# Performance work log

Hardware: AMD Instinct MI355X
Metric: run time of the kernel (lower is better)

## Reference

```python
import jax, jax.numpy as jnp
import numpy as np

N, F, P, NT = 4096, 256, 5, 5  # agents, feat dim, n_persona, n_time_steps
EPS = 1e-8


def setup_inputs() -> dict:
    key = jax.random.key(0)
    ks = jax.random.split(key, 7)
    attributes = jax.random.normal(ks[0], (N, F), dtype=jnp.float32)
    edges = (jax.random.uniform(ks[1], (N, N)) < 0.01).astype(jnp.float32)
    persona = jax.random.uniform(ks[2], (NT, N, P), dtype=jnp.float32)
    T = jax.random.uniform(ks[3], (P,), dtype=jnp.float32) * 0.5 + 0.5  # keep temperature away from 0
    e = jax.random.uniform(ks[4], (P,), dtype=jnp.float32) + 0.5
    r = jax.random.uniform(ks[5], (P,), dtype=jnp.float32)
    W = jax.random.uniform(ks[6], (P,), dtype=jnp.float32) + 0.5
    return {"attributes": attributes, "edges": edges, "persona": persona,
            "T": T, "e": e, "r": r, "W": W, "times": 2}


def reference(attributes, edges, persona, T, e, r, W, times):
    p = persona[times]                      # [N, P] persona weights at this time step
    msg = edges @ attributes                # [N, F] message passing, shared across personas

    def body(acc, xs):
        idx, Ti, ei, ri, Wi, pi = xs        # pi: [N]
        feat = ri * attributes + (msg * Wi) * (1.0 - ri)          # [N, F]
        nf = feat / jnp.sqrt(jnp.sum(feat * feat, axis=1, keepdims=True))  # row L2 norm
        x = jnp.exp((nf @ nf.T) / (Ti + EPS)) * ei                 # [N, N]
        x = x / (jnp.max(x) + EPS)                                 # min-max scale (min=0)
        # (1 - exp(-2v)) / (1 + exp(-2v)) == tanh(v)
        tc = jnp.tanh(x) * pi[None, :]                              # column persona gating
        # i == 0 initializes edges_prob with tc, every i adds row-gated tc
        acc = acc + tc * pi[:, None] + jnp.where(idx == 0, 1.0, 0.0) * tc
        return acc, None

    acc0 = jnp.zeros((N, N), dtype=jnp.float32)
    out, _ = jax.lax.scan(body, acc0, (jnp.arange(P), T, e, r, W, p.T))
    return out
```

## Files before the change

### kernel.cpp

```cpp
#include <hip/hip_runtime.h>
#include <hip/hip_bf16.h>

#define N 4096
#define F 256
#define P 5
#define EPSV 1e-8f
#define BK 32
#define NSTEP (F / BK)
#define NTRI 2080
#define GRIDSZ 512
#define DDEG 12
#define NC (DDEG + 1)

typedef __attribute__((ext_vector_type(8))) short bf16x8;
typedef __attribute__((ext_vector_type(4))) float f32x4;
typedef __attribute__((ext_vector_type(2))) float f32x2;

__device__ __forceinline__ f32x4 mfma16(bf16x8 a, bf16x8 b, f32x4 c) {
    return __builtin_amdgcn_mfma_f32_16x16x32_bf16(a, b, c, 0, 0, 0);
}

__device__ __forceinline__ void gload16(const void* src, const char* ldsdst) {
    __builtin_amdgcn_global_load_lds(
        (const __attribute__((address_space(1))) void*)src,
        (__attribute__((address_space(3))) void*)ldsdst, 16, 0, 0);
}

__device__ __forceinline__ f32x2 sp(float x) { return (f32x2){x, x}; }

__global__ __launch_bounds__(256, 8) void prep_kernel(
    const float* __restrict__ E, const float* __restrict__ A,
    const float* __restrict__ persona,
    const float* __restrict__ Tt, const float* __restrict__ ee,
    const float* __restrict__ rr, const float* __restrict__ Ww,
    const int* __restrict__ times,
    __hip_bfloat16* __restrict__ Abf, __hip_bfloat16* __restrict__ Mbf,
    float* __restrict__ qsoa, float* __restrict__ cstg, int* __restrict__ ctr) {
    __shared__ int cnt;
    __shared__ int list[1024];
    const int a = blockIdx.x;
    const int t = threadIdx.x;
    if (t == 0) cnt = 0;
    __syncthreads();
    const float4* erow = (const float4*)(E + (size_t)a * N);
    for (int b = t; b < N / 4; b += 256) {
        const float4 v = erow[b];
        if (v.x != 0.f) list[atomicAdd(&cnt, 1)] = 4 * b;
        if (v.y != 0.f) list[atomicAdd(&cnt, 1)] = 4 * b + 1;
        if (v.z != 0.f) list[atomicAdd(&cnt, 1)] = 4 * b + 2;
        if (v.w != 0.f) list[atomicAdd(&cnt, 1)] = 4 * b + 3;
    }
    __syncthreads();
    const int c = cnt;
    float s0 = 0.f, s1 = 0.f, s2 = 0.f, s3 = 0.f;
    float s4 = 0.f, s5 = 0.f, s6 = 0.f, s7 = 0.f;
    int j = 0;
    for (; j + 8 <= c; j += 8) {
        s0 += A[(size_t)list[j] * F + t];
        s1 += A[(size_t)list[j + 1] * F + t];
        s2 += A[(size_t)list[j + 2] * F + t];
        s3 += A[(size_t)list[j + 3] * F + t];
        s4 += A[(size_t)list[j + 4] * F + t];
        s5 += A[(size_t)list[j + 5] * F + t];
        s6 += A[(size_t)list[j + 6] * F + t];
        s7 += A[(size_t)list[j + 7] * F + t];
    }
    for (; j < c; ++j) s0 += A[(size_t)list[j] * F + t];
    const float mv = ((s0 + s1) + (s2 + s3)) + ((s4 + s5) + (s6 + s7));
    const float av = A[(size_t)a * F + t];
    Abf[(size_t)a * F + t] = __float2bfloat16(av);
    Mbf[(size_t)a * F + t] = __float2bfloat16(mv);

    float paa = av * av, pam = av * mv, pmm = mv * mv;
    #pragma unroll
    for (int o = 32; o > 0; o >>= 1) {
        paa += __shfl_down(paa, o);
        pam += __shfl_down(pam, o);
        pmm += __shfl_down(pmm, o);
    }
    __shared__ float s[3][4];
    const int wid = t >> 6;
    if ((t & 63) == 0) { s[0][wid] = paa; s[1][wid] = pam; s[2][wid] = pmm; }
    __syncthreads();
    if (t < P) {
        const float naa = s[0][0] + s[0][1] + s[0][2] + s[0][3];
        const float nam = s[1][0] + s[1][1] + s[1][2] + s[1][3];
        const float nmm = s[2][0] + s[2][1] + s[2][2] + s[2][3];
        const float Ti = Tt[t], ei = ee[t], ri = rr[t], Wi = Ww[t];
        const float wb = (1.f - ri) * Wi;
        const float n2 = ri * ri * naa + 2.f * ri * wb * nam + wb * wb * nmm;
        const float rn = rsqrtf(n2);
        const float p = persona[(size_t)(*times) * (size_t)N * P + (size_t)a * P + t];
        qsoa[(t * 4 + 0) * N + a] = ri * rn;
        qsoa[(t * 4 + 1) * N + a] = wb * rn;
        qsoa[(t * 4 + 2) * N + a] = p;
        qsoa[(t * 4 + 3) * N + a] = p + (t == 0 ? 1.f : 0.f);
        if (a == 0) {
            const float kk = 1.f / (Ti + EPSV);
            const float scf = ei / (ei * __expf(kk) + EPSV);
            float ch[NC];
            #pragma unroll
            for (int j2 = 0; j2 < NC; ++j2) ch[j2] = 0.f;
            for (int m = 0; m < 32; ++m) {
                const float th = 3.14159265358979323846f * (m + 0.5f) / 32.f;
                const float c1 = __cosf(th);
                const float x = scf * __expf(kk * 1.05f * c1);
                const float e2 = __expf(2.f * x);
                const float fm = 1.f - 2.f / (e2 + 1.f);
                float cjm1 = 1.f, cj = c1;
                ch[0] += fm;
                ch[1] += fm * c1;
                #pragma unroll
                for (int j2 = 2; j2 < NC; ++j2) {
                    const float cn = 2.f * c1 * cj - cjm1;
                    ch[j2] += fm * cn;
                    cjm1 = cj;
                    cj = cn;
                }
            }
            #pragma unroll
            for (int j2 = 0; j2 < NC; ++j2) ch[j2] *= (j2 == 0 ? 1.f : 2.f) / 32.f;
            float mono[NC], Tp[NC], Tc[NC], Tn[NC];
            const float is = 1.f / 1.05f;
            #pragma unroll
            for (int k2 = 0; k2 < NC; ++k2) {
                mono[k2] = 0.f; Tp[k2] = 0.f; Tc[k2] = 0.f; Tn[k2] = 0.f;
            }
            Tp[0] = 1.f;
            Tc[1] = is;
            #pragma unroll
            for (int k2 = 0; k2 < NC; ++k2) mono[k2] += ch[0] * Tp[k2] + ch[1] * Tc[k2];
            for (int j2 = 2; j2 < NC; ++j2) {
                #pragma unroll
                for (int k2 = 0; k2 < NC; ++k2)
                    Tn[k2] = 2.f * is * (k2 ? Tc[k2 - 1] : 0.f) - Tp[k2];
                #pragma unroll
                for (int k2 = 0; k2 < NC; ++k2) mono[k2] += ch[j2] * Tn[k2];
                #pragma unroll
                for (int k2 = 0; k2 < NC; ++k2) { Tp[k2] = Tc[k2]; Tc[k2] = Tn[k2]; }
            }
            #pragma unroll
            for (int k2 = 0; k2 < NC; ++k2) cstg[t * NC + k2] = mono[k2];
        }
    }
    if (a == 0 && t == 0) *ctr = GRIDSZ;
}

__global__ __launch_bounds__(512) void gram_kernel(
    const __hip_bfloat16* __restrict__ Abf, const __hip_bfloat16* __restrict__ Mbf,
    const float* __restrict__ qsoa, const float* __restrict__ cstg,
    int* __restrict__ ctr, float* __restrict__ out) {
    __shared__ __align__(16) char smem[43280];
    __shared__ int snext;

    const int t = threadIdx.x;
    const int lane = t & 63;
    const int w = t >> 6;
    const int wr = w >> 1;
    const int wc = w & 1;

    const int sslot = (lane & 3) ^ ((lane >> 3) & 3);
    const int srowoff = (w & 1) * 32 + (lane >> 2);
    const int ldsp = (w >> 1) * 4096 + (w & 1) * 2048;
    const __hip_bfloat16* smat = ((w >> 1) & 1) ? Mbf : Abf;

    const int frow = lane & 15;
    const int fg = lane >> 4;
    const int jr = fg << 2;
    const int rdslot = (fg ^ ((frow >> 1) & 3)) << 4;
    const int aoff = (wr * 16 + frow) * 64 + rdslot;
    const int coff0 = (wc * 32 + frow) * 64 + rdslot;
    const int coff1 = (wc * 32 + 16 + frow) * 64 + rdslot;

    const float* qlr = (const float*)(smem + 32768);
    const float* qlc = (const float*)(smem + 37888);
    const float* cfs = (const float*)(smem + 43008);

    int raw = blockIdx.x;
    while (raw < NTRI) {
        const int bid = (raw & 7) * 260 + (raw >> 3);
        int bx = (int)((sqrtf(8.f * (float)bid + 1.f) - 1.f) * 0.5f);
        while ((bx + 1) * (bx + 2) / 2 <= bid) ++bx;
        while (bx * (bx + 1) / 2 > bid) --bx;
        const int by = bid - bx * (bx + 1) / 2;
        const int row0 = by << 6, col0 = bx << 6;

        const int sbase = (w < 4) ? row0 : col0;
        const __hip_bfloat16* psrc =
            smat + (size_t)(sbase + srowoff) * F + sslot * 8;

        #define STAGE(b, ks)  do {                                        \
            const char* lb_ = smem + (b) * 16384 + ldsp;                  \
            gload16(psrc + (ks), lb_);                                    \
            gload16(psrc + (ks) + 16 * F, lb_ + 1024);                    \
        } while (0)

        __syncthreads();
        STAGE(0, 0);
        if (w == 0) {
            #pragma unroll
            for (int it = 0; it < 5; ++it)
                gload16(qsoa + (it * 4 + (lane >> 4)) * N + row0 + (lane & 15) * 4,
                        smem + 32768 + it * 1024);
        } else if (w == 1) {
            #pragma unroll
            for (int it = 0; it < 5; ++it)
                gload16(qsoa + (it * 4 + (lane >> 4)) * N + col0 + (lane & 15) * 4,
                        smem + 37888 + it * 1024);
        } else if (w == 2) {
            if (lane < 17) gload16(cstg + lane * 4, smem + 43008);
        }
        if (t == 0) snext = atomicAdd(ctr, 1);
        __syncthreads();

        f32x4 acc[4][2];
        #pragma unroll
        for (int g = 0; g < 4; ++g)
            #pragma unroll
            for (int n = 0; n < 2; ++n) acc[g][n] = (f32x4){0.f, 0.f, 0.f, 0.f};

        for (int s = 0; s < NSTEP; ++s) {
            const int b = s & 1;
            if (s + 1 < NSTEP) STAGE(b ^ 1, (s + 1) * BK);
            const char* base = smem + b * 16384;
            const bf16x8 aA = *(const bf16x8*)(base + aoff);
            const bf16x8 aM = *(const bf16x8*)(base + 4096 + aoff);
            const bf16x8 bA0 = *(const bf16x8*)(base + 8192 + coff0);
            const bf16x8 bA1 = *(const bf16x8*)(base + 8192 + coff1);
            const bf16x8 bM0 = *(const bf16x8*)(base + 12288 + coff0);
            const bf16x8 bM1 = *(const bf16x8*)(base + 12288 + coff1);
            acc[0][0] = mfma16(aA, bA0, acc[0][0]);
            acc[0][1] = mfma16(aA, bA1, acc[0][1]);
            acc[1][0] = mfma16(aA, bM0, acc[1][0]);
            acc[1][1] = mfma16(aA, bM1, acc[1][1]);
            acc[2][0] = mfma16(aM, bA0, acc[2][0]);
            acc[2][1] = mfma16(aM, bA1, acc[2][1]);
            acc[3][0] = mfma16(aM, bM0, acc[3][0]);
            acc[3][1] = mfma16(aM, bM1, acc[3][1]);
            if (s + 1 < NSTEP) __syncthreads();
        }

        f32x2 o1[2][2], o2[2][2];
        #pragma unroll
        for (int n = 0; n < 2; ++n)
            #pragma unroll
            for (int jp = 0; jp < 2; ++jp) { o1[n][jp] = sp(0.f); o2[n][jp] = sp(0.f); }

        #pragma unroll
        for (int i = 0; i < P; ++i) {
            const int ib = i * 256;
            float cf[NC];
            #pragma unroll
            for (int k = 0; k < NC; ++k) cf[k] = cfs[i * NC + k];
            float cA[2], cB[2], cP0[2], cP1[2];
            #pragma unroll
            for (int n = 0; n < 2; ++n) {
                const int cr = wc * 32 + n * 16 + frow;
                cA[n]  = qlc[ib + cr];
                cB[n]  = qlc[ib + 64 + cr];
                cP0[n] = qlc[ib + 128 + cr];
                cP1[n] = qlc[ib + 192 + cr];
            }
            #pragma unroll
            for (int jp = 0; jp < 2; ++jp) {
                const int rrw = wr * 16 + jr + jp * 2;
                const f32x2 rA  = *(const f32x2*)&qlr[ib + rrw];
                const f32x2 rB  = *(const f32x2*)&qlr[ib + 64 + rrw];
                const f32x2 rP0 = *(const f32x2*)&qlr[ib + 128 + rrw];
                const f32x2 rP1 = *(const f32x2*)&qlr[ib + 192 + rrw];
                #pragma unroll
                for (int n = 0; n < 2; ++n) {
                    const f32x2 aAA = (f32x2){acc[0][n][2 * jp], acc[0][n][2 * jp + 1]};
                    const f32x2 aAM = (f32x2){acc[1][n][2 * jp], acc[1][n][2 * jp + 1]};
                    const f32x2 aMA = (f32x2){acc[2][n][2 * jp], acc[2][n][2 * jp + 1]};
                    const f32x2 aMM = (f32x2){acc[3][n][2 * jp], acc[3][n][2 * jp + 1]};
                    const f32x2 h0 = rA * aAA + rB * aMA;
                    const f32x2 h1 = rA * aAM + rB * aMM;
                    const f32x2 g2 = h0 * sp(cA[n]) + h1 * sp(cB[n]);
                    f32x2 f2 = sp(cf[DDEG]);
                    #pragma unroll
                    for (int k = DDEG - 1; k >= 0; --k) f2 = f2 * g2 + sp(cf[k]);
                    o1[n][jp] += (f2 * rP1) * sp(cP0[n]);
                    o2[n][jp] += (f2 * rP0) * sp(cP1[n]);
                }
            }
        }

        #pragma unroll
        for (int jp = 0; jp < 2; ++jp)
            #pragma unroll
            for (int cc = 0; cc < 2; ++cc) {
                const int gr = row0 + wr * 16 + jr + jp * 2 + cc;
                #pragma unroll
                for (int n = 0; n < 2; ++n) {
                    const int gc = col0 + wc * 32 + n * 16 + frow;
                    out[(size_t)gr * N + gc] = o1[n][jp][cc];
                }
            }
        if (by != bx) {
            #pragma unroll
            for (int jp = 0; jp < 2; ++jp)
                #pragma unroll
                for (int cc = 0; cc < 2; ++cc) {
                    const int gr = row0 + wr * 16 + jr + jp * 2 + cc;
                    #pragma unroll
                    for (int n = 0; n < 2; ++n) {
                        const int gc = col0 + wc * 32 + n * 16 + frow;
                        out[(size_t)gc * N + gr] = o2[n][jp][cc];
                    }
                }
        }
        raw = snext;
        #undef STAGE
    }
}

extern "C" void kernel_launch(void* const* d_in, const int* in_sizes, int n_in,
                              void* d_out, int out_size, void* d_ws, size_t ws_size,
                              hipStream_t stream) {
    const float* A = (const float*)d_in[0];
    const float* E = (const float*)d_in[1];
    const float* persona = (const float*)d_in[2];
    const float* T = (const float*)d_in[3];
    const float* e = (const float*)d_in[4];
    const float* r = (const float*)d_in[5];
    const float* W = (const float*)d_in[6];
    const int* times = (const int*)d_in[7];
    float* out = (float*)d_out;

    char* ws = (char*)d_ws;
    __hip_bfloat16* Abf = (__hip_bfloat16*)ws;
    __hip_bfloat16* Mbf = (__hip_bfloat16*)(ws + (2 << 20));
    float* qsoa = (float*)(ws + (4 << 20));
    float* cstg = (float*)(ws + (4 << 20) + 5 * 4 * N * 4);
    int* ctr = (int*)(ws + (4 << 20) + 5 * 4 * N * 4 + 512);

    prep_kernel<<<N, 256, 0, stream>>>(E, A, persona, T, e, r, W, times,
                                       Abf, Mbf, qsoa, cstg, ctr);
    gram_kernel<<<GRIDSZ, 512, 0, stream>>>(Abf, Mbf, qsoa, cstg, ctr, out);
}
```

Measured before the change: 89.09 us.

## Triple-buffer K loop and prefetch next tile during epilogue in persistent gram kernel

Moves the bf16 panel staging from a double buffer to a three-stage ring, so two k-steps are in flight. It replaces __syncthreads with explicit vmcnt waits plus raw s_barrier. It also issues the next tile's first loads and its q-vector loads (double-buffered by parity) before the current tile's epilogue, overlapping global latency with the tanh/polynomial compute and the stores. The aim is to hide load latency between tiles, at the cost of more LDS (about 70KB, which lowers occupancy) and fragile hand-counted vmcnt values that must match the outstanding stores.

```diff
diff --git a/kernel.cpp b/kernel.cpp
--- a/kernel.cpp
+++ b/kernel.cpp
@@ -11,6 +11,10 @@
 #define GRIDSZ 512
 #define DDEG 12
 #define NC (DDEG + 1)
+#define PAN 16384
+#define Q0OFF 49152
+#define QSZ 10240
+#define CFOFF 69632
 
 typedef __attribute__((ext_vector_type(8))) short bf16x8;
 typedef __attribute__((ext_vector_type(4))) float f32x4;
@@ -27,6 +31,9 @@
 }
 
 __device__ __forceinline__ f32x2 sp(float x) { return (f32x2){x, x}; }
+
+#define SB() __builtin_amdgcn_sched_barrier(0)
+#define RAWBAR() do { SB(); __builtin_amdgcn_s_barrier(); SB(); } while (0)
 
 __global__ __launch_bounds__(256, 8) void prep_kernel(
     const float* __restrict__ E, const float* __restrict__ A,
@@ -150,7 +157,7 @@
     const __hip_bfloat16* __restrict__ Abf, const __hip_bfloat16* __restrict__ Mbf,
     const float* __restrict__ qsoa, const float* __restrict__ cstg,
     int* __restrict__ ctr, float* __restrict__ out) {
-    __shared__ __align__(16) char smem[43280];
+    __shared__ __align__(16) char smem[69904];
     __shared__ int snext;
 
     const int t = threadIdx.x;
@@ -171,47 +178,61 @@
     const int aoff = (wr * 16 + frow) * 64 + rdslot;
     const int coff0 = (wc * 32 + frow) * 64 + rdslot;
     const int coff1 = (wc * 32 + 16 + frow) * 64 + rdslot;
-
-    const float* qlr = (const float*)(smem + 32768);
-    const float* qlc = (const float*)(smem + 37888);
-    const float* cfs = (const float*)(smem + 43008);
+    const float* cfs = (const float*)(smem + CFOFF);
+
+    #define DECODE(id, oby, obx) do {                                     \
+        const int bid_ = ((id) & 7) * 260 + ((id) >> 3);                  \
+        int bx_ = (int)((sqrtf(8.f * (float)bid_ + 1.f) - 1.f) * 0.5f);   \
+        while ((bx_ + 1) * (bx_ + 2) / 2 <= bid_) ++bx_;                  \
+        while (bx_ * (bx_ + 1) / 2 > bid_) --bx_;                         \
+        (obx) = bx_;                                                      \
+        (oby) = bid_ - bx_ * (bx_ + 1) / 2;                               \
+    } while (0)
+
+    #define PROLOGUE(r0_, c0_, qp_) do {                                  \
+        const int sb_ = (w < 4) ? (r0_) : (c0_);                          \
+        const __hip_bfloat16* ps_ =                                       \
+            smat + (size_t)(sb_ + srowoff) * F + sslot * 8;               \
+        gload16(ps_, smem + ldsp);                                        \
+        gload16(ps_ + 16 * F, smem + ldsp + 1024);                        \
+        gload16(ps_ + 32, smem + PAN + ldsp);                             \
+        gload16(ps_ + 32 + 16 * F, smem + PAN + ldsp + 1024);             \
+        const int qb_ = Q0OFF + (qp_) * QSZ;                              \
+        if (w == 0) {                                                     \
+            _Pragma("unroll")                                             \
+            for (int it = 0; it < 5; ++it)                                \
+                gload16(qsoa + (it * 4 + (lane >> 4)) * N + (r0_) +       \
+                        (lane & 15) * 4, smem + qb_ + it * 1024);         \
+        } else if (w == 1) {                                              \
+            _Pragma("unroll")                                             \
+            for (int it = 0; it < 5; ++it)                                \
+                gload16(qsoa + (it * 4 + (lane >> 4)) * N + (c0_) +       \
+                        (lane & 15) * 4, smem + qb_ + 5120 + it * 1024);  \
+        }                                                                 \
+        if (t == 0) snext = atomicAdd(ctr, 1);                            \
+    } while (0)
 
     int raw = blockIdx.x;
-    while (raw < NTRI) {
-        const int bid = (raw & 7) * 260 + (raw >> 3);
-        int bx = (int)((sqrtf(8.f * (float)bid + 1.f) - 1.f) * 0.5f);
-        while ((bx + 1) * (bx + 2) / 2 <= bid) ++bx;
-        while (bx * (bx + 1) / 2 > bid) --bx;
-        const int by = bid - bx * (bx + 1) / 2;
-        const int row0 = by << 6, col0 = bx << 6;
-
-        const int sbase = (w < 4) ? row0 : col0;
+    int by, bx;
+    DECODE(raw, by, bx);
+    int row0 = by << 6, col0 = bx << 6;
+    int qpar = 0;
+    int pend = 0;
+
+    PROLOGUE(row0, col0, 0);
+    if (w == 2 && lane < 17) gload16(cstg + lane * 4, smem + CFOFF);
+
+    for (;;) {
+        if (pend == 16) asm volatile("s_waitcnt vmcnt(16)" ::: "memory");
+        else if (pend == 8) asm volatile("s_waitcnt vmcnt(8)" ::: "memory");
+        else asm volatile("s_waitcnt vmcnt(0)" ::: "memory");
+        RAWBAR();
+
+        const int nxt = snext;
+
+        const int sbc = (w < 4) ? row0 : col0;
         const __hip_bfloat16* psrc =
-            smat + (size_t)(sbase + srowoff) * F + sslot * 8;
-
-        #define STAGE(b, ks)  do {                                        \
-            const char* lb_ = smem + (b) * 16384 + ldsp;                  \
-            gload16(psrc + (ks), lb_);                                    \
-            gload16(psrc + (ks) + 16 * F, lb_ + 1024);                    \
-        } while (0)
-
-        __syncthreads();
-        STAGE(0, 0);
-        if (w == 0) {
-            #pragma unroll
-            for (int it = 0; it < 5; ++it)
-                gload16(qsoa + (it * 4 + (lane >> 4)) * N + row0 + (lane & 15) * 4,
-                        smem + 32768 + it * 1024);
-        } else if (w == 1) {
-            #pragma unroll
-            for (int it = 0; it < 5; ++it)
-                gload16(qsoa + (it * 4 + (lane >> 4)) * N + col0 + (lane & 15) * 4,
-                        smem + 37888 + it * 1024);
-        } else if (w == 2) {
-            if (lane < 17) gload16(cstg + lane * 4, smem + 43008);
-        }
-        if (t == 0) snext = atomicAdd(ctr, 1);
-        __syncthreads();
+            smat + (size_t)(sbc + srowoff) * F + sslot * 8;
 
         f32x4 acc[4][2];
         #pragma unroll
@@ -219,10 +240,14 @@
             #pragma unroll
             for (int n = 0; n < 2; ++n) acc[g][n] = (f32x4){0.f, 0.f, 0.f, 0.f};
 
+        #pragma unroll
         for (int s = 0; s < NSTEP; ++s) {
-            const int b = s & 1;
-            if (s + 1 < NSTEP) STAGE(b ^ 1, (s + 1) * BK);
-            const char* base = smem + b * 16384;
+            if (s + 2 < NSTEP) {
+                const char* lb = smem + ((s + 2) % 3) * PAN + ldsp;
+                gload16(psrc + (s + 2) * BK, lb);
+                gload16(psrc + (s + 2) * BK + 16 * F, lb + 1024);
+            }
+            const char* base = smem + (s % 3) * PAN;
             const bf16x8 aA = *(const bf16x8*)(base + aoff);
             const bf16x8 aM = *(const bf16x8*)(base + 4096 + aoff);
             const bf16x8 bA0 = *(const bf16x8*)(base + 8192 + coff0);
@@ -237,9 +262,26 @@
             acc[2][1] = mfma16(aM, bA1, acc[2][1]);
             acc[3][0] = mfma16(aM, bM0, acc[3][0]);
             acc[3][1] = mfma16(aM, bM1, acc[3][1]);
-            if (s + 1 < NSTEP) __syncthreads();
-        }
-
+            if (s + 1 < NSTEP) {
+                if (s + 2 < NSTEP) asm volatile("s_waitcnt vmcnt(2)" ::: "memory");
+                else asm volatile("s_waitcnt vmcnt(0)" ::: "memory");
+                RAWBAR();
+            }
+        }
+
+        RAWBAR();
+
+        const bool have = (nxt < NTRI);
+        int nby = 0, nbx = 0, nrow0 = 0, ncol0 = 0;
+        if (have) {
+            DECODE(nxt, nby, nbx);
+            nrow0 = nby << 6;
+            ncol0 = nbx << 6;
+            PROLOGUE(nrow0, ncol0, qpar ^ 1);
+        }
+
+        const float* qlr = (const float*)(smem + Q0OFF + qpar * QSZ);
+        const float* qlc = qlr + 1280;
         f32x2 o1[2][2], o2[2][2];
         #pragma unroll
         for (int n = 0; n < 2; ++n)
@@ -309,10 +351,16 @@
                         out[(size_t)gc * N + gr] = o2[n][jp][cc];
                     }
                 }
-        }
-        raw = snext;
-        #undef STAGE
-    }
+            pend = 16;
+        } else {
+            pend = 8;
+        }
+
+        if (!have) break;
+        raw = nxt; by = nby; bx = nbx; row0 = nrow0; col0 = ncol0; qpar ^= 1;
+    }
+    #undef PROLOGUE
+    #undef DECODE
 }
 
 extern "C" void kernel_launch(void* const* d_in, const int* in_sizes, int n_in,
```

Measured after the change: 80.73 us. 9.4% less time.
